# Kernel tuning notes

Hardware: AMD Instinct MI355X
Metric: run time of the kernel (lower is better)

Reference implementation:

```python
import jax, jax.numpy as jnp
import numpy as np

S, N, F_IN, F_OUT = 8, 4096, 128, 128


def setup_inputs() -> dict:
    key = jax.random.key(0)
    ks = jax.random.split(key, 7)
    return {
        "theta": jax.random.normal(ks[0], (S,), dtype=jnp.float32),
        "T_slices": jax.random.normal(ks[1], (S, N, N), dtype=jnp.float32),
        "x": jax.random.normal(ks[2], (N, F_IN), dtype=jnp.float32),
        "a": jax.random.uniform(ks[3], (N, N), dtype=jnp.float32),
        "W_fc": jax.random.normal(ks[4], (F_OUT, F_IN), dtype=jnp.float32) * (1.0 / np.sqrt(F_IN)),
        "b_fc": jax.random.normal(ks[5], (F_OUT,), dtype=jnp.float32) * 0.01,
        "prelu_alpha": jnp.full((F_IN,), 0.25, dtype=jnp.float32),
    }


def reference(theta, T_slices, x, a, W_fc, b_fc, prelu_alpha):
    # q = sum_s theta[s] * T_slices[s]  -> [N, N]
    q = jnp.einsum("s,snm->nm", theta, T_slices)
    # mask by adjacency (the torch code then converts to sparse; math is identical)
    q = q * a
    # diffused features: [N, N] @ [N, F_in] -> [N, F_in]
    out = q @ x
    # per-channel PReLU over the feature dim (num_parameters = input_dim)
    out = jnp.where(out >= 0, out, prelu_alpha * out)
    # final linear: out @ W_fc.T + b_fc -> [N, F_out]
    return out @ W_fc.T + b_fc
```

## Files before the change

kernel.cpp:

```cpp
#include <hip/hip_runtime.h>
#include <stdint.h>

constexpr int N  = 4096;
constexpr int F  = 128;
constexpr int S  = 8;
constexpr int BM = 32;
constexpr int KSPLIT = 8;
constexpr int KRANGE = N / KSPLIT;
constexpr int BK = 32;
constexpr int NCH = KRANGE / BK;
constexpr int NT = 256;

typedef float f4  __attribute__((ext_vector_type(4)));
typedef short bf16x8 __attribute__((ext_vector_type(8)));
typedef unsigned short us4 __attribute__((ext_vector_type(4)));

__device__ __forceinline__ unsigned short f2bf(float f) {
  union { float f; unsigned int u; } v; v.f = f;
  unsigned int u = v.u + 0x7FFFu + ((v.u >> 16) & 1u);
  return (unsigned short)(u >> 16);
}

__device__ __forceinline__ void bar_sync() {
  asm volatile("s_waitcnt lgkmcnt(0)" ::: "memory");
  __builtin_amdgcn_s_barrier();
  asm volatile("" ::: "memory");
}

__device__ __forceinline__ void vm_drain() {
  asm volatile("s_waitcnt vmcnt(0)" ::: "memory");
}

__device__ __forceinline__ void gload_lds16(const void* g, void* l) {
  __builtin_amdgcn_global_load_lds(
      (const __attribute__((address_space(1))) void*)g,
      (__attribute__((address_space(3))) void*)l, 16, 0, 0);
}

__global__ __launch_bounds__(256, 2) void ggd_xt(
    const float* __restrict__ x, unsigned short* __restrict__ xT) {
  __shared__ float xl[64][132];
  const int t  = threadIdx.x;
  const int k0 = blockIdx.x * 64;

  {
    const int kr = t >> 2, fs = (t & 3) * 32;
    const float* src = x + (size_t)(k0 + kr) * F + fs;
#pragma unroll
    for (int i = 0; i < 8; ++i)
      *(f4*)&xl[kr][fs + i * 4] = *(const f4*)(src + i * 4);
  }
  __syncthreads();
  {
    const int f = t >> 1, kh = (t & 1) * 32;
    us4 o[8];
#pragma unroll
    for (int i = 0; i < 32; ++i)
      o[i >> 2][i & 3] = f2bf(xl[kh + i][f]);
    unsigned short* dst = xT + (size_t)f * N + k0 + kh;
#pragma unroll
    for (int j = 0; j < 8; ++j)
      *(us4*)(dst + j * 4) = o[j];
  }
}

template <bool USE_WS>
__global__ __launch_bounds__(NT, 2) void ggd_diffuse(
    const float* __restrict__ theta,
    const float* __restrict__ Ts,
    const unsigned short* __restrict__ xT,
    const float* __restrict__ a,
    float* __restrict__ dst)
{
  __shared__ float rawT[S][BM][BK];
  __shared__ float rawA[BM][BK];
  __shared__ unsigned short xt_lds[2][F][BK];
  __shared__ unsigned short q_lds[BM][BK];

  const int t  = threadIdx.x;
  const int rb = blockIdx.x >> 3;
  const int ks = blockIdx.x & 7;
  const int n0 = rb * BM;
  const int k0 = ks * KRANGE;

  float th[S];
#pragma unroll
  for (int s = 0; s < S; ++s) th[s] = theta[s];

  const int wave = t >> 6, lane = t & 63;

  const int grow = lane >> 3;
  const int gcol = (lane & 7) * 4;
  const size_t slice = (size_t)N * N;

  const int qr = t >> 3;
  const int qk = (t & 7) * 4;

  const int rtile = wave >> 1;
  const int fbase = (wave & 1) * 4;

  f4 acc[4];
#pragma unroll
  for (int i = 0; i < 4; ++i) acc[i] = (f4)(0.f);

  auto stage_raw = [&](int c) {
    const size_t cb = (size_t)(k0 + c * BK) + gcol;
#pragma unroll
    for (int j = 0; j < 8; ++j) {
      const int i = wave * 8 + j;
      const int s = i >> 2;
      const int q4 = i & 3;
      const float* src = Ts + (size_t)s * slice +
                         (size_t)(n0 + q4 * 8 + grow) * N + cb;
      gload_lds16(src, (float*)&rawT[0][0][0] + i * 256);
    }
    {
      const float* src = a + (size_t)(n0 + wave * 8 + grow) * N + cb;
      gload_lds16(src, (float*)&rawA[0][0] + wave * 256);
    }
  };

  auto stage_x = [&](int c, int buf) {
    const uint8_t* xb = (const uint8_t*)xT;
    const size_t kbyte = (size_t)(k0 + c * BK) * 2;
#pragma unroll
    for (int j = 0; j < 2; ++j) {
      const int i = wave * 2 + j;
      const int fr = i * 16 + (lane >> 2);
      const uint8_t* src = xb + (size_t)fr * (N * 2) + kbyte + (lane & 3) * 16;
      gload_lds16(src, &xt_lds[buf][i * 16][0]);
    }
  };

  auto qgen = [&]() {
    f4 av = *(const f4*)&rawA[qr][qk];
    f4 sum;
    {
      f4 tv = *(const f4*)&rawT[0][qr][qk];
#pragma unroll
      for (int j = 0; j < 4; ++j) sum[j] = th[0] * tv[j];
    }
#pragma unroll
    for (int s = 1; s < S; ++s) {
      f4 tv = *(const f4*)&rawT[s][qr][qk];
#pragma unroll
      for (int j = 0; j < 4; ++j) sum[j] = fmaf(th[s], tv[j], sum[j]);
    }
    us4 q;
#pragma unroll
    for (int j = 0; j < 4; ++j) q[j] = f2bf(av[j] * sum[j]);
    *(us4*)&q_lds[qr][qk] = q;
  };

  auto compute = [&](int buf) {
    const unsigned short* qb = &q_lds[rtile * 16][0];
    bf16x8 afrag = *(const bf16x8*)(qb + (lane & 15) * BK + (lane >> 4) * 8);
#pragma unroll
    for (int i = 0; i < 4; ++i) {
      const int ftile = fbase + i;
      const unsigned short* bb = &xt_lds[buf][ftile * 16][0];
      bf16x8 bfrag = *(const bf16x8*)(bb + (lane & 15) * BK + (lane >> 4) * 8);
      acc[i] = __builtin_amdgcn_mfma_f32_16x16x32_bf16(afrag, bfrag, acc[i],
                                                       0, 0, 0);
    }
  };

  stage_raw(0);
  stage_x(0, 0);
  vm_drain();
  bar_sync();
  qgen();
  bar_sync();

  for (int c = 0; c < NCH; ++c) {
    const int buf = c & 1;
    const bool more = (c + 1 < NCH);
    if (more) {
      stage_raw(c + 1);
      stage_x(c + 1, buf ^ 1);
    }
    compute(buf);
    if (more) {
      vm_drain();
      bar_sync();
      qgen();
      bar_sync();
    }
  }

  const int crow = n0 + rtile * 16 + (lane >> 4) * 4;
  const int ccol = (lane & 15);
#pragma unroll
  for (int i = 0; i < 4; ++i) {
    const int fo = (fbase + i) * 16 + ccol;
#pragma unroll
    for (int r = 0; r < 4; ++r) {
      const size_t row = (size_t)(crow + r);
      if (USE_WS) {
        dst[((size_t)ks * N + row) * F + fo] = acc[i][r];
      } else {
        atomicAdd(dst + row * F + fo, acc[i][r]);
      }
    }
  }
}

template <bool USE_WS>
__global__ __launch_bounds__(256, 2) void ggd_fc(
    const float* __restrict__ W,
    const float* __restrict__ bfc,
    const float* __restrict__ alpha,
    const float* __restrict__ src,
    float* __restrict__ out)
{
  __shared__ float p_lds[16 * F];
  const int t  = threadIdx.x;
  const int n0 = blockIdx.x * 16;

  {
    const int lr = t >> 4, c8 = (t & 15) * 8;
    f4 v0, v1;
    if (USE_WS) {
      v0 = (f4)(0.f); v1 = (f4)(0.f);
#pragma unroll
      for (int ks = 0; ks < KSPLIT; ++ks) {
        const float* sp = src + ((size_t)ks * N + n0 + lr) * F + c8;
        v0 += *(const f4*)(sp);
        v1 += *(const f4*)(sp + 4);
      }
    } else {
      const float* ip = src + (size_t)(n0 + lr) * F + c8;
      v0 = *(const f4*)(ip);
      v1 = *(const f4*)(ip + 4);
    }
    f4 a0 = *(const f4*)(alpha + c8);
    f4 a1 = *(const f4*)(alpha + c8 + 4);
#pragma unroll
    for (int j = 0; j < 4; ++j) {
      v0[j] = v0[j] >= 0.f ? v0[j] : a0[j] * v0[j];
      v1[j] = v1[j] >= 0.f ? v1[j] : a1[j] * v1[j];
    }
    *(f4*)&p_lds[lr * F + c8]     = v0;
    *(f4*)&p_lds[lr * F + c8 + 4] = v1;
  }
  __syncthreads();

  const int r2  = t >> 5;
  const int fo0 = (t & 31) * 4;
  f4 accA = *(const f4*)(bfc + fo0);
  f4 accB = accA;
#pragma unroll 4
  for (int fi4 = 0; fi4 < F / 4; ++fi4) {
    f4 pA = *(const f4*)&p_lds[r2 * F + fi4 * 4];
    f4 pB = *(const f4*)&p_lds[(r2 + 8) * F + fi4 * 4];
#pragma unroll
    for (int e = 0; e < 4; ++e) {
      f4 wv = *(const f4*)(W + (size_t)(fo0 + e) * F + fi4 * 4);
      accA[e] = fmaf(pA[0], wv[0], fmaf(pA[1], wv[1],
                fmaf(pA[2], wv[2], fmaf(pA[3], wv[3], accA[e]))));
      accB[e] = fmaf(pB[0], wv[0], fmaf(pB[1], wv[1],
                fmaf(pB[2], wv[2], fmaf(pB[3], wv[3], accB[e]))));
    }
  }
  *(f4*)(out + (size_t)(n0 + r2) * F + fo0)     = accA;
  *(f4*)(out + (size_t)(n0 + r2 + 8) * F + fo0) = accB;
}

extern "C" void kernel_launch(void* const* d_in, const int* in_sizes, int n_in,
                              void* d_out, int out_size, void* d_ws, size_t ws_size,
                              hipStream_t stream) {
  const float* theta = (const float*)d_in[0];
  const float* Ts    = (const float*)d_in[1];
  const float* x     = (const float*)d_in[2];
  const float* a     = (const float*)d_in[3];
  const float* W     = (const float*)d_in[4];
  const float* bfc   = (const float*)d_in[5];
  const float* alpha = (const float*)d_in[6];
  float* out = (float*)d_out;

  const size_t part_bytes = (size_t)KSPLIT * N * F * sizeof(float);
  const size_t xt_bytes   = (size_t)N * F * 2;
  if (ws_size >= part_bytes + xt_bytes && d_ws != nullptr) {
    float* parts = (float*)d_ws;
    unsigned short* xT = (unsigned short*)((char*)d_ws + part_bytes);
    ggd_xt<<<dim3(N / 64), dim3(256), 0, stream>>>(x, xT);
    ggd_diffuse<true><<<dim3((N / BM) * KSPLIT), dim3(NT), 0, stream>>>(
        theta, Ts, xT, a, parts);
    ggd_fc<true><<<dim3(N / 16), dim3(256), 0, stream>>>(
        W, bfc, alpha, parts, out);
  } else {
    unsigned short* xT = (unsigned short*)d_ws;
    hipMemsetAsync(out, 0, (size_t)out_size * sizeof(float), stream);
    ggd_xt<<<dim3(N / 64), dim3(256), 0, stream>>>(x, xT);
    ggd_diffuse<false><<<dim3((N / BM) * KSPLIT), dim3(NT), 0, stream>>>(
        theta, Ts, xT, a, out);
    ggd_fc<false><<<dim3(N / 16), dim3(256), 0, stream>>>(
        W, bfc, alpha, out, out);
  }
}
```

Measured before the change: 142.6 us.

## Halve diffuse row tile and deepen prefetch to two chunks ahead

Shrinks the diffusion block row tile from 32 to 16 rows and restructures the main loop to prefetch two chunks ahead, with double-buffered T staging, triple-buffered x tiles and double-buffered q tiles. A partial vmcnt wait replaces the full drain so newer loads stay in flight during q generation. The adjacency values now go straight from global memory into registers instead of through LDS. The aim is to hide global-load latency on the memory-bound T stream and launch more blocks, at the cost of more LDS per row of output and twice as many blocks issuing atomics or workspace writes.

New measurement: 147.2 us. +3.2%, slower.

```diff
diff --git a/kernel.cpp b/kernel.cpp
--- a/kernel.cpp
+++ b/kernel.cpp
@@ -4,7 +4,7 @@
 constexpr int N  = 4096;
 constexpr int F  = 128;
 constexpr int S  = 8;
-constexpr int BM = 32;
+constexpr int BM = 16;
 constexpr int KSPLIT = 8;
 constexpr int KRANGE = N / KSPLIT;
 constexpr int BK = 32;
@@ -12,6 +12,7 @@
 constexpr int NT = 256;
 
 typedef float f4  __attribute__((ext_vector_type(4)));
+typedef float f2  __attribute__((ext_vector_type(2)));
 typedef short bf16x8 __attribute__((ext_vector_type(8)));
 typedef unsigned short us4 __attribute__((ext_vector_type(4)));
 
@@ -29,6 +30,10 @@
 
 __device__ __forceinline__ void vm_drain() {
   asm volatile("s_waitcnt vmcnt(0)" ::: "memory");
+}
+
+__device__ __forceinline__ void vm_wait7() {
+  asm volatile("s_waitcnt vmcnt(7)" ::: "memory");
 }
 
 __device__ __forceinline__ void gload_lds16(const void* g, void* l) {
@@ -72,10 +77,9 @@
     const float* __restrict__ a,
     float* __restrict__ dst)
 {
-  __shared__ float rawT[S][BM][BK];
-  __shared__ float rawA[BM][BK];
-  __shared__ unsigned short xt_lds[2][F][BK];
-  __shared__ unsigned short q_lds[BM][BK];
+  __shared__ float rawT[2][S][BM][BK];
+  __shared__ unsigned short xt_lds[3][F][BK];
+  __shared__ unsigned short q_lds[2][BM][BK];
 
   const int t  = threadIdx.x;
   const int rb = blockIdx.x >> 3;
@@ -88,35 +92,25 @@
   for (int s = 0; s < S; ++s) th[s] = theta[s];
 
   const int wave = t >> 6, lane = t & 63;
-
-  const int grow = lane >> 3;
-  const int gcol = (lane & 7) * 4;
   const size_t slice = (size_t)N * N;
 
-  const int qr = t >> 3;
-  const int qk = (t & 7) * 4;
-
-  const int rtile = wave >> 1;
-  const int fbase = (wave & 1) * 4;
-
-  f4 acc[4];
-#pragma unroll
-  for (int i = 0; i < 4; ++i) acc[i] = (f4)(0.f);
-
-  auto stage_raw = [&](int c) {
-    const size_t cb = (size_t)(k0 + c * BK) + gcol;
-#pragma unroll
-    for (int j = 0; j < 8; ++j) {
-      const int i = wave * 8 + j;
-      const int s = i >> 2;
-      const int q4 = i & 3;
-      const float* src = Ts + (size_t)s * slice +
-                         (size_t)(n0 + q4 * 8 + grow) * N + cb;
-      gload_lds16(src, (float*)&rawT[0][0][0] + i * 256);
-    }
-    {
-      const float* src = a + (size_t)(n0 + wave * 8 + grow) * N + cb;
-      gload_lds16(src, (float*)&rawA[0][0] + wave * 256);
+  const int qr = t >> 4;
+  const int qk = (t & 15) * 2;
+
+  f4 acc[2];
+#pragma unroll
+  for (int i = 0; i < 2; ++i) acc[i] = (f4)(0.f);
+
+  auto stage_rawT = [&](int c, int buf) {
+    const size_t cb = (size_t)(k0 + c * BK) + (lane & 7) * 4;
+    const int grow = lane >> 3;
+#pragma unroll
+    for (int j = 0; j < 4; ++j) {
+      const int i = wave * 4 + j;
+      const int s = i >> 1;
+      const int row = (i & 1) * 8 + grow;
+      const float* src = Ts + (size_t)s * slice + (size_t)(n0 + row) * N + cb;
+      gload_lds16(src, &rawT[buf][0][0][0] + i * 256);
     }
   };
 
@@ -132,67 +126,79 @@
     }
   };
 
-  auto qgen = [&]() {
-    f4 av = *(const f4*)&rawA[qr][qk];
-    f4 sum;
+  auto load_a = [&](int c) -> f2 {
+    return *(const f2*)(a + (size_t)(n0 + qr) * N + (k0 + c * BK + qk));
+  };
+
+  auto qgen = [&](int c1, f2 av) {
+    const float* rt = &rawT[c1 & 1][0][qr][qk];
+    f2 sum;
     {
-      f4 tv = *(const f4*)&rawT[0][qr][qk];
-#pragma unroll
-      for (int j = 0; j < 4; ++j) sum[j] = th[0] * tv[j];
+      f2 tv = *(const f2*)(rt);
+      sum[0] = th[0] * tv[0];
+      sum[1] = th[0] * tv[1];
     }
 #pragma unroll
     for (int s = 1; s < S; ++s) {
-      f4 tv = *(const f4*)&rawT[s][qr][qk];
-#pragma unroll
-      for (int j = 0; j < 4; ++j) sum[j] = fmaf(th[s], tv[j], sum[j]);
-    }
-    us4 q;
-#pragma unroll
-    for (int j = 0; j < 4; ++j) q[j] = f2bf(av[j] * sum[j]);
-    *(us4*)&q_lds[qr][qk] = q;
-  };
-
-  auto compute = [&](int buf) {
-    const unsigned short* qb = &q_lds[rtile * 16][0];
-    bf16x8 afrag = *(const bf16x8*)(qb + (lane & 15) * BK + (lane >> 4) * 8);
-#pragma unroll
-    for (int i = 0; i < 4; ++i) {
-      const int ftile = fbase + i;
-      const unsigned short* bb = &xt_lds[buf][ftile * 16][0];
-      bf16x8 bfrag = *(const bf16x8*)(bb + (lane & 15) * BK + (lane >> 4) * 8);
-      acc[i] = __builtin_amdgcn_mfma_f32_16x16x32_bf16(afrag, bfrag, acc[i],
-                                                       0, 0, 0);
-    }
-  };
-
-  stage_raw(0);
+      f2 tv = *(const f2*)(rt + (size_t)s * (BM * BK));
+      sum[0] = fmaf(th[s], tv[0], sum[0]);
+      sum[1] = fmaf(th[s], tv[1], sum[1]);
+    }
+    const unsigned int packed =
+        (unsigned int)f2bf(av[0] * sum[0]) |
+        ((unsigned int)f2bf(av[1] * sum[1]) << 16);
+    *(unsigned int*)&q_lds[c1 & 1][qr][qk] = packed;
+  };
+
+  auto compute = [&](int c) {
+    const unsigned short* qb = &q_lds[c & 1][0][0];
+    bf16x8 af = *(const bf16x8*)(qb + (lane & 15) * BK + (lane >> 4) * 8);
+    const unsigned short* xb = &xt_lds[c % 3][0][0];
+#pragma unroll
+    for (int i = 0; i < 2; ++i) {
+      const int ft = wave * 2 + i;
+      bf16x8 bf = *(const bf16x8*)(xb + (size_t)(ft * 16 + (lane & 15)) * BK +
+                                   (lane >> 4) * 8);
+      acc[i] = __builtin_amdgcn_mfma_f32_16x16x32_bf16(af, bf, acc[i], 0, 0, 0);
+    }
+  };
+
+  f2 avE, avO;
+  stage_rawT(0, 0);
   stage_x(0, 0);
+  avE = load_a(0);
+  stage_rawT(1, 1);
+  stage_x(1, 1);
+  avO = load_a(1);
   vm_drain();
   bar_sync();
-  qgen();
+  qgen(0, avE);
   bar_sync();
 
-  for (int c = 0; c < NCH; ++c) {
-    const int buf = c & 1;
-    const bool more = (c + 1 < NCH);
-    if (more) {
-      stage_raw(c + 1);
-      stage_x(c + 1, buf ^ 1);
-    }
-    compute(buf);
-    if (more) {
-      vm_drain();
-      bar_sync();
-      qgen();
-      bar_sync();
-    }
-  }
-
-  const int crow = n0 + rtile * 16 + (lane >> 4) * 4;
-  const int ccol = (lane & 15);
-#pragma unroll
-  for (int i = 0; i < 4; ++i) {
-    const int fo = (fbase + i) * 16 + ccol;
+  auto body = [&](int c, f2& av_iss, f2 av_use) {
+    const bool iss = (c + 2 < NCH);
+    if (iss) {
+      stage_rawT(c + 2, c & 1);
+      stage_x(c + 2, (c + 2) % 3);
+      av_iss = load_a(c + 2);
+    }
+    compute(c);
+    if (iss) vm_wait7(); else vm_drain();
+    bar_sync();
+    if (c + 1 < NCH) qgen(c + 1, av_use);
+    bar_sync();
+  };
+
+  for (int cc = 0; cc < NCH; cc += 2) {
+    body(cc,     avE, avO);
+    body(cc + 1, avO, avE);
+  }
+
+  const int crow = n0 + (lane >> 4) * 4;
+  const int ccol = lane & 15;
+#pragma unroll
+  for (int i = 0; i < 2; ++i) {
+    const int fo = (wave * 2 + i) * 16 + ccol;
 #pragma unroll
     for (int r = 0; r < 4; ++r) {
       const size_t row = (size_t)(crow + r);
```
